# Optimization experiments

Measured on AMD Instinct MI355X. Metric: run time of the kernel, lower is better.

Reference implementation:

```python
import jax, jax.numpy as jnp
import numpy as np

N = 50000      # nodes
E = 800000     # edges (before self-loops)
IN = 256       # in_channels
OUT = 64       # out_channels per head
H = 4          # heads (layer 0)
LEAKY = 0.2    # PyG GATConv negative_slope default


def setup_inputs() -> dict:
    key = jax.random.key(0)
    ks = jax.random.split(key, 16)
    g = 0.1
    inp = {
        "x": jax.random.normal(ks[0], (N, IN), jnp.float32),
        "edge_index": jax.random.randint(ks[1], (2, E), 0, N, dtype=jnp.int32),
        # layer 0: in -> H*OUT, concat=True
        "W0": jax.random.normal(ks[2], (IN, H * OUT), jnp.float32) * g,
        "a_src0": jax.random.normal(ks[3], (H, OUT), jnp.float32) * g,
        "a_dst0": jax.random.normal(ks[4], (H, OUT), jnp.float32) * g,
        "b0": jnp.zeros((H * OUT,), jnp.float32),
        # layer 1: H*OUT -> OUT, heads=1, concat=False
        "W1": jax.random.normal(ks[5], (H * OUT, OUT), jnp.float32) * g,
        "a_src1": jax.random.normal(ks[6], (1, OUT), jnp.float32) * g,
        "a_dst1": jax.random.normal(ks[7], (1, OUT), jnp.float32) * g,
        "b1": jnp.zeros((OUT,), jnp.float32),
        # layer 2: H*OUT -> OUT (input is OUT from layer 1? no: layer1 outputs OUT)
        "W2": jax.random.normal(ks[8], (OUT, OUT), jnp.float32) * g,
        "a_src2": jax.random.normal(ks[9], (1, OUT), jnp.float32) * g,
        "a_dst2": jax.random.normal(ks[10], (1, OUT), jnp.float32) * g,
        "b2": jnp.zeros((OUT,), jnp.float32),
    }
    return inp


def _gat_layer(x, src, dst, W, a_s, a_d, b, heads, concat):
    """PyG GATConv: per-head linear, edge attention logits, segment softmax
    over incoming edges of each destination node, scatter-sum aggregate."""
    n = x.shape[0]
    h = (x @ W).reshape(n, heads, -1)                      # [N, H, C]
    al_s = (h * a_s).sum(-1)                               # [N, H]
    al_d = (h * a_d).sum(-1)                               # [N, H]
    e = jax.nn.leaky_relu(al_s[src] + al_d[dst], LEAKY)    # [E', H]
    m = jax.ops.segment_max(e, dst, num_segments=n)        # [N, H]
    ex = jnp.exp(e - m[dst])
    den = jax.ops.segment_sum(ex, dst, num_segments=n)     # [N, H]
    alpha = ex / (den[dst] + 1e-16)                        # [E', H]
    out = jax.ops.segment_sum(alpha[:, :, None] * h[src], dst, num_segments=n)  # [N,H,C]
    out = out.reshape(n, -1) if concat else out.mean(axis=1)
    return out + b


def reference(x, edge_index, W0, a_src0, a_dst0, b0, W1, a_src1, a_dst1, b1,
              W2, a_src2, a_dst2, b2):
    n = x.shape[0]
    loop = jnp.arange(n, dtype=edge_index.dtype)
    src = jnp.concatenate([edge_index[0], loop])   # PyG add_self_loops=True
    dst = jnp.concatenate([edge_index[1], loop])
    h = _gat_layer(x, src, dst, W0, a_src0, a_dst0, b0, H, True)
    h = jax.nn.elu(h)
    h = _gat_layer(h, src, dst, W1, a_src1, a_dst1, b1, 1, False)
    h = jax.nn.elu(h)
    h = _gat_layer(h, src, dst, W2, a_src2, a_dst2, b2, 1, False)
    h = jax.nn.elu(h)
    return h
```

## Files before the change

### kernel.cpp

```cpp
#include <hip/hip_runtime.h>
#include <hip/hip_bf16.h>


typedef unsigned short ushort_t;
typedef __attribute__((ext_vector_type(8))) short short8;
typedef __attribute__((ext_vector_type(4))) float f32x4;

__device__ __forceinline__ float elu_f(float x){ return x > 0.f ? x : expm1f(x); }
__device__ __forceinline__ float lrelu_f(float x){ return x > 0.f ? x : 0.2f * x; }
__device__ __forceinline__ ushort_t f2b(float f){
  union { float f; unsigned u; } v; v.f = f;
  unsigned r = v.u + 0x7fff + ((v.u >> 16) & 1);
  return (ushort_t)(r >> 16);
}
__device__ __forceinline__ float b2f_lo(unsigned v){
  union { unsigned u; float f; } c; c.u = v << 16; return c.f;
}
__device__ __forceinline__ float b2f_hi(unsigned v){
  union { unsigned u; float f; } c; c.u = v & 0xffff0000u; return c.f;
}

__global__ __launch_bounds__(256) void prep_kernel(const int* __restrict__ ei,
                                                   int* __restrict__ cnt,
                                                   const float4* __restrict__ x4,
                                                   ushort4* __restrict__ xb4, int n4,
                                                   const float* __restrict__ W0,
                                                   ushort_t* __restrict__ W0p,
                                                   const float* __restrict__ W1,
                                                   ushort_t* __restrict__ W1p,
                                                   const float* __restrict__ W2,
                                                   ushort_t* __restrict__ W2p,
                                                   int E, int Etot, int eb, int fb){
  int bid = blockIdx.x; int t = threadIdx.x;
  if(bid < eb){
    int e = bid * 256 + t;
    if(e < Etot){
      int d = (e < E) ? ei[E + e] : (e - E);
      atomicAdd(&cnt[d], 1);
    }
  } else if(bid < eb + fb){
    int i = (bid - eb) * 256 + t;
    if(i < n4){
      float4 v = x4[i];
      ushort4 o;
      o.x = f2b(v.x); o.y = f2b(v.y); o.z = f2b(v.z); o.w = f2b(v.w);
      xb4[i] = o;
    }
  } else {
    int r = bid - eb - fb;
    if(r < 256){
      int i = r * 256 + t; int k = i >> 8, n = i & 255;
      W0p[(size_t)n * 256 + k] = f2b(W0[i]);
    } else if(r < 320){
      int i = (r - 256) * 256 + t; int k = i >> 6, n = i & 63;
      W1p[(size_t)n * 256 + k] = f2b(W1[i]);
    } else {
      int i = (r - 320) * 256 + t; int k = i >> 6, n = i & 63;
      W2p[(size_t)n * 64 + k] = f2b(W2[i]);
    }
  }
}

#define SKP 264
__global__ __launch_bounds__(256) void gemm0_kernel(const ushort_t* __restrict__ A,
                                                    const ushort_t* __restrict__ Bp,
                                                    ushort_t* __restrict__ h0b,
                                                    const float* __restrict__ asrc,
                                                    const float* __restrict__ adst,
                                                    float* __restrict__ als,
                                                    float* __restrict__ ald, int M){
  __shared__ ushort_t As[32 * SKP];
  int t = threadIdx.x;
  int row0 = blockIdx.x * 32;
  {
    int c = t;
    #pragma unroll
    for(int it = 0; it < 4; it++, c += 256){
      int r = c >> 5;
      int kc = (c & 31) << 3;
      int gr = row0 + r;
      short8 v = {};
      if(gr < M) v = *(const short8*)(A + (size_t)gr * 256 + kc);
      *(short8*)(As + r * SKP + kc) = v;
    }
  }
  __syncthreads();
  int wave = t >> 6, lane = t & 63;
  int m = lane & 15, q = lane >> 4;
  int colb = wave;
  const ushort_t* Bq = Bp + (size_t)(colb * 64 + m) * 256 + q * 8;
  const ushort_t* A0 = As + m * SKP + q * 8;
  const ushort_t* A1 = As + (16 + m) * SKP + q * 8;
  f32x4 acc[2][4] = {};
  for(int k0 = 0; k0 < 256; k0 += 32){
    short8 bv[4];
    #pragma unroll
    for(int j = 0; j < 4; j++) bv[j] = *(const short8*)(Bq + (size_t)j * 16 * 256 + k0);
    short8 a0 = *(const short8*)(A0 + k0);
    short8 a1 = *(const short8*)(A1 + k0);
    #pragma unroll
    for(int j = 0; j < 4; j++){
      acc[0][j] = __builtin_amdgcn_mfma_f32_16x16x32_bf16(a0, bv[j], acc[0][j], 0, 0, 0);
      acc[1][j] = __builtin_amdgcn_mfma_f32_16x16x32_bf16(a1, bv[j], acc[1][j], 0, 0, 0);
    }
  }
  #pragma unroll
  for(int rt = 0; rt < 2; rt++){
    #pragma unroll
    for(int j = 0; j < 4; j++){
      int col = colb * 64 + j * 16 + m;
      #pragma unroll
      for(int i = 0; i < 4; i++){
        int gr = row0 + rt * 16 + q * 4 + i;
        if(gr < M) h0b[(size_t)gr * 256 + col] = f2b(acc[rt][j][i]);
      }
    }
    float vs[4] = {0,0,0,0}, vd[4] = {0,0,0,0};
    #pragma unroll
    for(int j = 0; j < 4; j++){
      int col = colb * 64 + j * 16 + m;
      float a_s = asrc[col], a_d = adst[col];
      #pragma unroll
      for(int i = 0; i < 4; i++){
        vs[i] = fmaf(acc[rt][j][i], a_s, vs[i]);
        vd[i] = fmaf(acc[rt][j][i], a_d, vd[i]);
      }
    }
    #pragma unroll
    for(int off = 8; off > 0; off >>= 1){
      #pragma unroll
      for(int i = 0; i < 4; i++){
        vs[i] += __shfl_down(vs[i], off, 16);
        vd[i] += __shfl_down(vd[i], off, 16);
      }
    }
    if(m == 0){
      #pragma unroll
      for(int i = 0; i < 4; i++){
        int gr = row0 + rt * 16 + q * 4 + i;
        if(gr < M){
          als[(size_t)gr * 4 + colb] = vs[i];
          ald[(size_t)gr * 4 + colb] = vd[i];
        }
      }
    }
  }
}

__global__ __launch_bounds__(256) void blocksum_kernel(const int* __restrict__ cnt,
                                                       int* __restrict__ bsum, int N){
  __shared__ int sm[256];
  int t = threadIdx.x;
  int i = blockIdx.x * 256 + t;
  sm[t] = (i < N) ? cnt[i] : 0;
  __syncthreads();
  for(int off = 128; off > 0; off >>= 1){
    if(t < off) sm[t] += sm[t + off];
    __syncthreads();
  }
  if(t == 0) bsum[blockIdx.x] = sm[0];
}

__global__ __launch_bounds__(256) void scanb_kernel(int* __restrict__ bsum, int nb){
  __shared__ int sm[256];
  int t = threadIdx.x;
  int v = (t < nb) ? bsum[t] : 0;
  sm[t] = v;
  __syncthreads();
  for(int off = 1; off < 256; off <<= 1){
    int x = 0;
    if(t >= off) x = sm[t - off];
    __syncthreads();
    sm[t] += x;
    __syncthreads();
  }
  if(t < nb) bsum[t] = sm[t] - v;
}

__global__ __launch_bounds__(256) void scan2_kernel(const int* __restrict__ cnt,
                                                    const int* __restrict__ bsum,
                                                    int* __restrict__ rowptr,
                                                    int* __restrict__ cursor,
                                                    int N, int Etot){
  __shared__ int sm[256];
  int t = threadIdx.x;
  int i = blockIdx.x * 256 + t;
  int v = (i < N) ? cnt[i] : 0;
  sm[t] = v;
  __syncthreads();
  for(int off = 1; off < 256; off <<= 1){
    int x = 0;
    if(t >= off) x = sm[t - off];
    __syncthreads();
    sm[t] += x;
    __syncthreads();
  }
  if(i < N){
    int ex = sm[t] - v + bsum[blockIdx.x];
    rowptr[i] = ex;
    cursor[i] = ex;
    if(i == N - 1) rowptr[N] = Etot;
  }
}

__global__ __launch_bounds__(256) void scatter_kernel(const int* __restrict__ ei,
                                                      int* __restrict__ cursor,
                                                      int* __restrict__ esrc,
                                                      int E, int Etot){
  int e = blockIdx.x * 256 + threadIdx.x;
  if(e >= Etot) return;
  int s, d;
  if(e < E){ s = ei[e]; d = ei[E + e]; } else { s = e - E; d = s; }
  int pos = atomicAdd(&cursor[d], 1);
  esrc[pos] = s;
}

#define H1S 264
__global__ __launch_bounds__(256) void agg0g1_kernel(const int* __restrict__ rowptr,
                                                     const int* __restrict__ esrc,
                                                     const uint2* __restrict__ h0b2,
                                                     const float* __restrict__ als,
                                                     const float* __restrict__ ald,
                                                     const float* __restrict__ b0,
                                                     const ushort_t* __restrict__ W1p,
                                                     const float* __restrict__ as1,
                                                     const float* __restrict__ ad1,
                                                     ushort_t* __restrict__ g1b,
                                                     float* __restrict__ als1,
                                                     float* __restrict__ ald1, int N){
  __shared__ ushort_t Hs[16 * H1S];
  __shared__ float aps[4][16], apd[4][16];
  int t = threadIdx.x;
  int wave = t >> 6, lane = t & 63;
  int nbase = blockIdx.x * 16;
  int h = lane >> 4;
  int mm16 = lane & 15;
  for(int j = 0; j < 4; j++){
    int n = nbase + wave * 4 + j;
    int nl = wave * 4 + j;
    if(n < N){
      int beg = rowptr[n], end = rowptr[n + 1];
      float adh = ald[(size_t)n * 4 + h];
      float4 acc = make_float4(0.f, 0.f, 0.f, 0.f);
      float den = 0.f;
      for(int c0 = beg; c0 < end; c0 += 16){
        int e = c0 + mm16;
        int s = n; float w = 0.f;
        if(e < end){
          s = esrc[e];
          w = expf(lrelu_f(als[(size_t)s * 4 + h] + adh));
        }
        #pragma unroll
        for(int i = 0; i < 16; i++){
          int idx = (lane & 48) + i;
          int si = __shfl(s, idx, 64);
          float wi = __shfl(w, idx, 64);
          uint2 v = h0b2[((size_t)si << 6) + lane];
          acc.x = fmaf(wi, b2f_lo(v.x), acc.x);
          acc.y = fmaf(wi, b2f_hi(v.x), acc.y);
          acc.z = fmaf(wi, b2f_lo(v.y), acc.z);
          acc.w = fmaf(wi, b2f_hi(v.y), acc.w);
          den += wi;
        }
      }
      float inv = 1.f / (den + 1e-16f);
      float4 bb = ((const float4*)b0)[lane];
      uint2 o;
      o.x = (unsigned)f2b(elu_f(acc.x * inv + bb.x)) |
            ((unsigned)f2b(elu_f(acc.y * inv + bb.y)) << 16);
      o.y = (unsigned)f2b(elu_f(acc.z * inv + bb.z)) |
            ((unsigned)f2b(elu_f(acc.w * inv + bb.w)) << 16);
      *(uint2*)(Hs + nl * H1S + lane * 4) = o;
    }
  }
  __syncthreads();
  int m = lane & 15, q = lane >> 4;
  const ushort_t* Bw = W1p + (size_t)(wave * 16 + m) * 256 + q * 8;
  const ushort_t* Aw = Hs + m * H1S + q * 8;
  f32x4 acc = {};
  #pragma unroll
  for(int k0 = 0; k0 < 256; k0 += 32){
    short8 av = *(const short8*)(Aw + k0);
    short8 bv = *(const short8*)(Bw + k0);
    acc = __builtin_amdgcn_mfma_f32_16x16x32_bf16(av, bv, acc, 0, 0, 0);
  }
  float a_s = as1[wave * 16 + m], a_d = ad1[wave * 16 + m];
  float vs[4], vd[4];
  #pragma unroll
  for(int i = 0; i < 4; i++){
    int gn = nbase + q * 4 + i;
    if(gn < N) g1b[(size_t)gn * 64 + wave * 16 + m] = f2b(acc[i]);
    vs[i] = acc[i] * a_s;
    vd[i] = acc[i] * a_d;
  }
  #pragma unroll
  for(int off = 8; off > 0; off >>= 1){
    #pragma unroll
    for(int i = 0; i < 4; i++){
      vs[i] += __shfl_down(vs[i], off, 16);
      vd[i] += __shfl_down(vd[i], off, 16);
    }
  }
  if(m == 0){
    #pragma unroll
    for(int i = 0; i < 4; i++){
      aps[wave][q * 4 + i] = vs[i];
      apd[wave][q * 4 + i] = vd[i];
    }
  }
  __syncthreads();
  if(t < 16){
    int gn = nbase + t;
    if(gn < N){
      als1[gn] = aps[0][t] + aps[1][t] + aps[2][t] + aps[3][t];
      ald1[gn] = apd[0][t] + apd[1][t] + apd[2][t] + apd[3][t];
    }
  }
}

#define H2S 72
__global__ __launch_bounds__(256) void agg1g2_kernel(const int* __restrict__ rowptr,
                                                     const int* __restrict__ esrc,
                                                     const unsigned* __restrict__ g1b,
                                                     const float* __restrict__ als1,
                                                     const float* __restrict__ ald1,
                                                     const float* __restrict__ b1,
                                                     const ushort_t* __restrict__ W2p,
                                                     const float* __restrict__ as2,
                                                     const float* __restrict__ ad2,
                                                     ushort_t* __restrict__ g2b,
                                                     float* __restrict__ als2,
                                                     float* __restrict__ ald2, int N){
  __shared__ ushort_t Hs[16 * H2S];
  __shared__ float aps[4][16], apd[4][16];
  int t = threadIdx.x;
  int wave = t >> 6, lane = t & 63;
  int nbase = blockIdx.x * 16;
  int half = lane >> 5;
  int p = lane & 31;
  for(int j = 0; j < 4; j++){
    int n = nbase + wave * 4 + j;
    int nl = wave * 4 + j;
    if(n < N){
      int beg = rowptr[n], end = rowptr[n + 1];
      float ad = ald1[n];
      float a0 = 0.f, a1 = 0.f, den = 0.f;
      for(int c0 = beg; c0 < end; c0 += 32){
        int e = c0 + p;
        int s = n; float w = 0.f;
        if(e < end){
          s = esrc[e];
          w = expf(lrelu_f(als1[s] + ad));
        }
        #pragma unroll
        for(int i = 0; i < 16; i++){
          int idx = 2 * i + half;
          int si = __shfl(s, idx, 64);
          float wi = __shfl(w, idx, 64);
          unsigned v = g1b[((size_t)si << 5) + p];
          a0 = fmaf(wi, b2f_lo(v), a0);
          a1 = fmaf(wi, b2f_hi(v), a1);
          den += wi;
        }
      }
      a0 += __shfl_xor(a0, 32, 64);
      a1 += __shfl_xor(a1, 32, 64);
      den += __shfl_xor(den, 32, 64);
      float inv = 1.f / (den + 1e-16f);
      float2 bb = ((const float2*)b1)[p];
      if(half == 0){
        unsigned o = (unsigned)f2b(elu_f(a0 * inv + bb.x)) |
                     ((unsigned)f2b(elu_f(a1 * inv + bb.y)) << 16);
        *(unsigned*)(Hs + nl * H2S + p * 2) = o;
      }
    }
  }
  __syncthreads();
  int m = lane & 15, q = lane >> 4;
  const ushort_t* Bw = W2p + (size_t)(wave * 16 + m) * 64 + q * 8;
  const ushort_t* Aw = Hs + m * H2S + q * 8;
  f32x4 acc = {};
  #pragma unroll
  for(int k0 = 0; k0 < 64; k0 += 32){
    short8 av = *(const short8*)(Aw + k0);
    short8 bv = *(const short8*)(Bw + k0);
    acc = __builtin_amdgcn_mfma_f32_16x16x32_bf16(av, bv, acc, 0, 0, 0);
  }
  float a_s = as2[wave * 16 + m], a_d = ad2[wave * 16 + m];
  float vs[4], vd[4];
  #pragma unroll
  for(int i = 0; i < 4; i++){
    int gn = nbase + q * 4 + i;
    if(gn < N) g2b[(size_t)gn * 64 + wave * 16 + m] = f2b(acc[i]);
    vs[i] = acc[i] * a_s;
    vd[i] = acc[i] * a_d;
  }
  #pragma unroll
  for(int off = 8; off > 0; off >>= 1){
    #pragma unroll
    for(int i = 0; i < 4; i++){
      vs[i] += __shfl_down(vs[i], off, 16);
      vd[i] += __shfl_down(vd[i], off, 16);
    }
  }
  if(m == 0){
    #pragma unroll
    for(int i = 0; i < 4; i++){
      aps[wave][q * 4 + i] = vs[i];
      apd[wave][q * 4 + i] = vd[i];
    }
  }
  __syncthreads();
  if(t < 16){
    int gn = nbase + t;
    if(gn < N){
      als2[gn] = aps[0][t] + aps[1][t] + aps[2][t] + aps[3][t];
      ald2[gn] = apd[0][t] + apd[1][t] + apd[2][t] + apd[3][t];
    }
  }
}

__global__ __launch_bounds__(256) void aggF_kernel(const int* __restrict__ rowptr,
                                                   const int* __restrict__ esrc,
                                                   const unsigned* __restrict__ gb,
                                                   const float* __restrict__ als,
                                                   const float* __restrict__ ald,
                                                   const float* __restrict__ b,
                                                   float2* __restrict__ outp, int N){
  int t = threadIdx.x;
  int lane = t & 63;
  int n = blockIdx.x * 4 + (t >> 6);
  if(n >= N) return;
  int half = lane >> 5;
  int p = lane & 31;
  int beg = rowptr[n], end = rowptr[n + 1];
  float ad = ald[n];
  float a0 = 0.f, a1 = 0.f, den = 0.f;
  for(int c0 = beg; c0 < end; c0 += 32){
    int e = c0 + p;
    int s = n; float w = 0.f;
    if(e < end){
      s = esrc[e];
      w = expf(lrelu_f(als[s] + ad));
    }
    #pragma unroll
    for(int i = 0; i < 16; i++){
      int idx = 2 * i + half;
      int si = __shfl(s, idx, 64);
      float wi = __shfl(w, idx, 64);
      unsigned v = gb[((size_t)si << 5) + p];
      a0 = fmaf(wi, b2f_lo(v), a0);
      a1 = fmaf(wi, b2f_hi(v), a1);
      den += wi;
    }
  }
  a0 += __shfl_xor(a0, 32, 64);
  a1 += __shfl_xor(a1, 32, 64);
  den += __shfl_xor(den, 32, 64);
  float inv = 1.f / (den + 1e-16f);
  float2 bb = ((const float2*)b)[p];
  if(half == 0){
    float2 o;
    o.x = elu_f(a0 * inv + bb.x);
    o.y = elu_f(a1 * inv + bb.y);
    outp[((size_t)n << 5) + p] = o;
  }
}

extern "C" void kernel_launch(void* const* d_in, const int* in_sizes, int n_in,
                              void* d_out, int out_size, void* d_ws, size_t ws_size,
                              hipStream_t stream){
  const float* x   = (const float*)d_in[0];
  const int*   ei  = (const int*)d_in[1];
  const float* W0  = (const float*)d_in[2];
  const float* as0 = (const float*)d_in[3];
  const float* ad0 = (const float*)d_in[4];
  const float* b0  = (const float*)d_in[5];
  const float* W1  = (const float*)d_in[6];
  const float* as1 = (const float*)d_in[7];
  const float* ad1 = (const float*)d_in[8];
  const float* b1  = (const float*)d_in[9];
  const float* W2  = (const float*)d_in[10];
  const float* as2 = (const float*)d_in[11];
  const float* ad2 = (const float*)d_in[12];
  const float* b2  = (const float*)d_in[13];
  int N = in_sizes[0] / 256;
  int E = in_sizes[1] / 2;
  int Etot = E + N;

  size_t off = 0;
  auto alc = [&](size_t bytes) -> char* {
    char* p = (char*)d_ws + off;
    off += (bytes + 255) & ~(size_t)255;
    return p;
  };
  ushort_t* xb    = (ushort_t*)alc((size_t)N * 256 * 2);
  ushort_t* h0b   = (ushort_t*)alc((size_t)N * 256 * 2);
  float*    als   = (float*)alc((size_t)N * 4 * 4);
  float*    ald   = (float*)alc((size_t)N * 4 * 4);
  float*    als1  = (float*)alc((size_t)N * 4);
  float*    ald1  = (float*)alc((size_t)N * 4);
  float*    als2  = (float*)alc((size_t)N * 4);
  float*    ald2  = (float*)alc((size_t)N * 4);
  int*      esrc  = (int*)alc((size_t)Etot * 4);
  int*      rowptr= (int*)alc((size_t)(N + 1) * 4);
  int*      cnt   = (int*)alc((size_t)N * 4);
  int*      cursor= (int*)alc((size_t)N * 4);
  int*      bsum  = (int*)alc(256 * 4);
  ushort_t* W0p   = (ushort_t*)alc(256 * 256 * 2);
  ushort_t* W1p   = (ushort_t*)alc(256 * 64 * 2);
  ushort_t* W2p   = (ushort_t*)alc(64 * 64 * 2);

  ushort_t* g1b = xb;
  ushort_t* g2b = h0b;

  int nb = (N + 255) / 256;
  int eb = (Etot + 255) / 256;
  int fb = (N * 64 + 255) / 256;
  int g0b = (N + 31) / 32;
  int tb = (N + 15) / 16;
  int ab = (N + 3) / 4;

  hipMemsetAsync(cnt, 0, (size_t)N * 4, stream);
  prep_kernel<<<eb + fb + 336, 256, 0, stream>>>(ei, cnt, (const float4*)x,
                                                 (ushort4*)xb, N * 64,
                                                 W0, W0p, W1, W1p, W2, W2p,
                                                 E, Etot, eb, fb);
  blocksum_kernel<<<nb, 256, 0, stream>>>(cnt, bsum, N);
  scanb_kernel<<<1, 256, 0, stream>>>(bsum, nb);
  scan2_kernel<<<nb, 256, 0, stream>>>(cnt, bsum, rowptr, cursor, N, Etot);
  scatter_kernel<<<eb, 256, 0, stream>>>(ei, cursor, esrc, E, Etot);

  gemm0_kernel<<<g0b, 256, 0, stream>>>(xb, W0p, h0b, as0, ad0, als, ald, N);

  agg0g1_kernel<<<tb, 256, 0, stream>>>(rowptr, esrc, (const uint2*)h0b,
                                        als, ald, b0, W1p, as1, ad1,
                                        g1b, als1, ald1, N);

  agg1g2_kernel<<<tb, 256, 0, stream>>>(rowptr, esrc, (const unsigned*)g1b,
                                        als1, ald1, b1, W2p, as2, ad2,
                                        g2b, als2, ald2, N);

  aggF_kernel<<<ab, 256, 0, stream>>>(rowptr, esrc, (const unsigned*)g2b,
                                      als2, ald2, b2, (float2*)d_out, N);
}
```

Baseline: 379.2 us.

## Merge graph-build stages into cooperative kernel and split layer-1 aggregation from GEMM

Replaces the memset, prep, blocksum, scan and scatter launches with a single cooperative kernel that uses grid-wide syncs between phases. It also splits the fused layer-0 aggregation plus layer-1 GEMM into two kernels: a one-node-per-wave aggregation that writes bf16 activations to global memory, and a standalone MFMA GEMM that computes the layer-1 attention logits. The aim is to cut launch overhead and give the aggregation better occupancy, without the shared-memory staging and block barriers. In exchange it adds a global round trip for the intermediate activations, plus grid-sync costs in a fixed 512-block grid.

```diff
diff --git a/kernel.cpp b/kernel.cpp
--- a/kernel.cpp
+++ b/kernel.cpp
@@ -1,5 +1,8 @@
 #include <hip/hip_runtime.h>
 #include <hip/hip_bf16.h>
+#include <hip/hip_cooperative_groups.h>
+
+namespace cg = cooperative_groups;
 
 
 typedef unsigned short ushort_t;
@@ -20,44 +23,99 @@
   union { unsigned u; float f; } c; c.u = v & 0xffff0000u; return c.f;
 }
 
-__global__ __launch_bounds__(256) void prep_kernel(const int* __restrict__ ei,
-                                                   int* __restrict__ cnt,
-                                                   const float4* __restrict__ x4,
-                                                   ushort4* __restrict__ xb4, int n4,
-                                                   const float* __restrict__ W0,
-                                                   ushort_t* __restrict__ W0p,
-                                                   const float* __restrict__ W1,
-                                                   ushort_t* __restrict__ W1p,
-                                                   const float* __restrict__ W2,
-                                                   ushort_t* __restrict__ W2p,
-                                                   int E, int Etot, int eb, int fb){
-  int bid = blockIdx.x; int t = threadIdx.x;
-  if(bid < eb){
-    int e = bid * 256 + t;
-    if(e < Etot){
-      int d = (e < E) ? ei[E + e] : (e - E);
-      atomicAdd(&cnt[d], 1);
-    }
-  } else if(bid < eb + fb){
-    int i = (bid - eb) * 256 + t;
-    if(i < n4){
-      float4 v = x4[i];
-      ushort4 o;
-      o.x = f2b(v.x); o.y = f2b(v.y); o.z = f2b(v.z); o.w = f2b(v.w);
-      xb4[i] = o;
-    }
-  } else {
-    int r = bid - eb - fb;
-    if(r < 256){
-      int i = r * 256 + t; int k = i >> 8, n = i & 255;
-      W0p[(size_t)n * 256 + k] = f2b(W0[i]);
-    } else if(r < 320){
-      int i = (r - 256) * 256 + t; int k = i >> 6, n = i & 63;
-      W1p[(size_t)n * 256 + k] = f2b(W1[i]);
-    } else {
-      int i = (r - 320) * 256 + t; int k = i >> 6, n = i & 63;
-      W2p[(size_t)n * 64 + k] = f2b(W2[i]);
-    }
+struct BuildArgs {
+  const int* ei; int* cnt;
+  const float4* x4; ushort4* xb4; int n4;
+  const float* W0; ushort_t* W0p;
+  const float* W1; ushort_t* W1p;
+  const float* W2; ushort_t* W2p;
+  int* bsum; int* rowptr; int* cursor; int* esrc;
+  int N, E, Etot, nb;
+};
+
+__global__ __launch_bounds__(256, 4) void build_kernel(BuildArgs p){
+  cg::grid_group grid = cg::this_grid();
+  __shared__ int sm[256];
+  int t = threadIdx.x;
+  int gid = blockIdx.x * 256 + t;
+  int gsz = gridDim.x * 256;
+  for(int i = gid; i < p.N; i += gsz) p.cnt[i] = 0;
+  for(int i = gid; i < p.n4; i += gsz){
+    float4 v = p.x4[i];
+    ushort4 o;
+    o.x = f2b(v.x); o.y = f2b(v.y); o.z = f2b(v.z); o.w = f2b(v.w);
+    p.xb4[i] = o;
+  }
+  for(int i = gid; i < 256 * 256; i += gsz){
+    int k = i >> 8, n = i & 255;
+    p.W0p[(size_t)n * 256 + k] = f2b(p.W0[i]);
+  }
+  for(int i = gid; i < 256 * 64; i += gsz){
+    int k = i >> 6, n = i & 63;
+    p.W1p[(size_t)n * 256 + k] = f2b(p.W1[i]);
+  }
+  for(int i = gid; i < 64 * 64; i += gsz){
+    int k = i >> 6, n = i & 63;
+    p.W2p[(size_t)n * 64 + k] = f2b(p.W2[i]);
+  }
+  grid.sync();
+  for(int e = gid; e < p.Etot; e += gsz){
+    int d = (e < p.E) ? p.ei[p.E + e] : (e - p.E);
+    atomicAdd(&p.cnt[d], 1);
+  }
+  grid.sync();
+  for(int c = blockIdx.x; c < p.nb; c += gridDim.x){
+    int i = c * 256 + t;
+    sm[t] = (i < p.N) ? p.cnt[i] : 0;
+    __syncthreads();
+    for(int off = 128; off > 0; off >>= 1){
+      if(t < off) sm[t] += sm[t + off];
+      __syncthreads();
+    }
+    if(t == 0) p.bsum[c] = sm[0];
+    __syncthreads();
+  }
+  grid.sync();
+  if(blockIdx.x == 0){
+    int v = (t < p.nb) ? p.bsum[t] : 0;
+    sm[t] = v;
+    __syncthreads();
+    for(int off = 1; off < 256; off <<= 1){
+      int x = 0;
+      if(t >= off) x = sm[t - off];
+      __syncthreads();
+      sm[t] += x;
+      __syncthreads();
+    }
+    if(t < p.nb) p.bsum[t] = sm[t] - v;
+  }
+  grid.sync();
+  for(int c = blockIdx.x; c < p.nb; c += gridDim.x){
+    int i = c * 256 + t;
+    int v = (i < p.N) ? p.cnt[i] : 0;
+    sm[t] = v;
+    __syncthreads();
+    for(int off = 1; off < 256; off <<= 1){
+      int x = 0;
+      if(t >= off) x = sm[t - off];
+      __syncthreads();
+      sm[t] += x;
+      __syncthreads();
+    }
+    if(i < p.N){
+      int ex = sm[t] - v + p.bsum[c];
+      p.rowptr[i] = ex;
+      p.cursor[i] = ex;
+    }
+    __syncthreads();
+  }
+  if(gid == 0) p.rowptr[p.N] = p.Etot;
+  grid.sync();
+  for(int e = gid; e < p.Etot; e += gsz){
+    int s, d;
+    if(e < p.E){ s = p.ei[e]; d = p.ei[p.E + e]; } else { s = e - p.E; d = s; }
+    int pos = atomicAdd(&p.cursor[d], 1);
+    p.esrc[pos] = s;
   }
 }
 
@@ -147,173 +205,125 @@
   }
 }
 
-__global__ __launch_bounds__(256) void blocksum_kernel(const int* __restrict__ cnt,
-                                                       int* __restrict__ bsum, int N){
-  __shared__ int sm[256];
+__global__ __launch_bounds__(256) void agg0_kernel(const int* __restrict__ rowptr,
+                                                   const int* __restrict__ esrc,
+                                                   const uint2* __restrict__ h0b2,
+                                                   const float4* __restrict__ als4,
+                                                   const float4* __restrict__ ald4,
+                                                   const float4* __restrict__ b4,
+                                                   uint2* __restrict__ out2, int N){
   int t = threadIdx.x;
-  int i = blockIdx.x * 256 + t;
-  sm[t] = (i < N) ? cnt[i] : 0;
-  __syncthreads();
-  for(int off = 128; off > 0; off >>= 1){
-    if(t < off) sm[t] += sm[t + off];
-    __syncthreads();
-  }
-  if(t == 0) bsum[blockIdx.x] = sm[0];
-}
-
-__global__ __launch_bounds__(256) void scanb_kernel(int* __restrict__ bsum, int nb){
-  __shared__ int sm[256];
-  int t = threadIdx.x;
-  int v = (t < nb) ? bsum[t] : 0;
-  sm[t] = v;
-  __syncthreads();
-  for(int off = 1; off < 256; off <<= 1){
-    int x = 0;
-    if(t >= off) x = sm[t - off];
-    __syncthreads();
-    sm[t] += x;
-    __syncthreads();
-  }
-  if(t < nb) bsum[t] = sm[t] - v;
-}
-
-__global__ __launch_bounds__(256) void scan2_kernel(const int* __restrict__ cnt,
-                                                    const int* __restrict__ bsum,
-                                                    int* __restrict__ rowptr,
-                                                    int* __restrict__ cursor,
-                                                    int N, int Etot){
-  __shared__ int sm[256];
-  int t = threadIdx.x;
-  int i = blockIdx.x * 256 + t;
-  int v = (i < N) ? cnt[i] : 0;
-  sm[t] = v;
-  __syncthreads();
-  for(int off = 1; off < 256; off <<= 1){
-    int x = 0;
-    if(t >= off) x = sm[t - off];
-    __syncthreads();
-    sm[t] += x;
-    __syncthreads();
-  }
-  if(i < N){
-    int ex = sm[t] - v + bsum[blockIdx.x];
-    rowptr[i] = ex;
-    cursor[i] = ex;
-    if(i == N - 1) rowptr[N] = Etot;
-  }
-}
-
-__global__ __launch_bounds__(256) void scatter_kernel(const int* __restrict__ ei,
-                                                      int* __restrict__ cursor,
-                                                      int* __restrict__ esrc,
-                                                      int E, int Etot){
-  int e = blockIdx.x * 256 + threadIdx.x;
-  if(e >= Etot) return;
-  int s, d;
-  if(e < E){ s = ei[e]; d = ei[E + e]; } else { s = e - E; d = s; }
-  int pos = atomicAdd(&cursor[d], 1);
-  esrc[pos] = s;
-}
-
-#define H1S 264
-__global__ __launch_bounds__(256) void agg0g1_kernel(const int* __restrict__ rowptr,
-                                                     const int* __restrict__ esrc,
-                                                     const uint2* __restrict__ h0b2,
-                                                     const float* __restrict__ als,
-                                                     const float* __restrict__ ald,
-                                                     const float* __restrict__ b0,
-                                                     const ushort_t* __restrict__ W1p,
-                                                     const float* __restrict__ as1,
-                                                     const float* __restrict__ ad1,
-                                                     ushort_t* __restrict__ g1b,
-                                                     float* __restrict__ als1,
-                                                     float* __restrict__ ald1, int N){
-  __shared__ ushort_t Hs[16 * H1S];
-  __shared__ float aps[4][16], apd[4][16];
-  int t = threadIdx.x;
-  int wave = t >> 6, lane = t & 63;
-  int nbase = blockIdx.x * 16;
+  int lane = t & 63;
+  int n = blockIdx.x * 4 + (t >> 6);
+  if(n >= N) return;
   int h = lane >> 4;
-  int mm16 = lane & 15;
-  for(int j = 0; j < 4; j++){
-    int n = nbase + wave * 4 + j;
-    int nl = wave * 4 + j;
-    if(n < N){
-      int beg = rowptr[n], end = rowptr[n + 1];
-      float adh = ald[(size_t)n * 4 + h];
-      float4 acc = make_float4(0.f, 0.f, 0.f, 0.f);
-      float den = 0.f;
-      for(int c0 = beg; c0 < end; c0 += 16){
-        int e = c0 + mm16;
-        int s = n; float w = 0.f;
-        if(e < end){
-          s = esrc[e];
-          w = expf(lrelu_f(als[(size_t)s * 4 + h] + adh));
-        }
-        #pragma unroll
-        for(int i = 0; i < 16; i++){
-          int idx = (lane & 48) + i;
-          int si = __shfl(s, idx, 64);
-          float wi = __shfl(w, idx, 64);
-          uint2 v = h0b2[((size_t)si << 6) + lane];
-          acc.x = fmaf(wi, b2f_lo(v.x), acc.x);
-          acc.y = fmaf(wi, b2f_hi(v.x), acc.y);
-          acc.z = fmaf(wi, b2f_lo(v.y), acc.z);
-          acc.w = fmaf(wi, b2f_hi(v.y), acc.w);
-          den += wi;
-        }
-      }
-      float inv = 1.f / (den + 1e-16f);
-      float4 bb = ((const float4*)b0)[lane];
-      uint2 o;
-      o.x = (unsigned)f2b(elu_f(acc.x * inv + bb.x)) |
-            ((unsigned)f2b(elu_f(acc.y * inv + bb.y)) << 16);
-      o.y = (unsigned)f2b(elu_f(acc.z * inv + bb.z)) |
-            ((unsigned)f2b(elu_f(acc.w * inv + bb.w)) << 16);
-      *(uint2*)(Hs + nl * H1S + lane * 4) = o;
-    }
-  }
-  __syncthreads();
+  int beg = rowptr[n], end = rowptr[n + 1];
+  float adh = ((const float*)(ald4 + n))[h];
+  float4 acc = make_float4(0.f, 0.f, 0.f, 0.f);
+  float den = 0.f;
+  for(int c0 = beg; c0 < end; c0 += 16){
+    int e = c0 + (lane & 15);
+    int s = n; float w = 0.f;
+    if(e < end){
+      s = esrc[e];
+      w = expf(lrelu_f(((const float*)(als4 + s))[h] + adh));
+    }
+    #pragma unroll
+    for(int i = 0; i < 16; i++){
+      int idx = (lane & 48) + i;
+      int si = __shfl(s, idx, 64);
+      float wi = __shfl(w, idx, 64);
+      uint2 v = h0b2[((size_t)si << 6) + lane];
+      acc.x = fmaf(wi, b2f_lo(v.x), acc.x);
+      acc.y = fmaf(wi, b2f_hi(v.x), acc.y);
+      acc.z = fmaf(wi, b2f_lo(v.y), acc.z);
+      acc.w = fmaf(wi, b2f_hi(v.y), acc.w);
+      den += wi;
+    }
+  }
+  float inv = 1.f / (den + 1e-16f);
+  float4 bb = b4[lane];
+  float v0 = elu_f(acc.x * inv + bb.x);
+  float v1 = elu_f(acc.y * inv + bb.y);
+  float v2 = elu_f(acc.z * inv + bb.z);
+  float v3 = elu_f(acc.w * inv + bb.w);
+  uint2 o;
+  o.x = (unsigned)f2b(v0) | ((unsigned)f2b(v1) << 16);
+  o.y = (unsigned)f2b(v2) | ((unsigned)f2b(v3) << 16);
+  out2[((size_t)n << 6) + lane] = o;
+}
+
+__global__ __launch_bounds__(256) void mfma_gemm(const ushort_t* __restrict__ A,
+                                                 const ushort_t* __restrict__ Bp,
+                                                 ushort_t* __restrict__ Cp,
+                                                 const float* __restrict__ asrc,
+                                                 const float* __restrict__ adst,
+                                                 float* __restrict__ als,
+                                                 float* __restrict__ ald,
+                                                 int M, int K, int NC){
+  int wave = threadIdx.x >> 6;
+  int lane = threadIdx.x & 63;
+  int tile0 = (blockIdx.x * 4 + wave) * 2;
+  if(tile0 * 16 >= M) return;
+  bool two = (tile0 + 1) * 16 < M;
   int m = lane & 15, q = lane >> 4;
-  const ushort_t* Bw = W1p + (size_t)(wave * 16 + m) * 256 + q * 8;
-  const ushort_t* Aw = Hs + m * H1S + q * 8;
-  f32x4 acc = {};
+  const ushort_t* Ab = A + (size_t)(tile0 * 16 + m) * K + q * 8;
+  const ushort_t* Bq = Bp + (size_t)m * K + q * 8;
+  f32x4 acc[2][4] = {};
+  for(int k0 = 0; k0 < K; k0 += 32){
+    short8 bv[4];
+    #pragma unroll
+    for(int j = 0; j < 4; j++) bv[j] = *(const short8*)(Bq + (size_t)j * 16 * K + k0);
+    short8 a0 = *(const short8*)(Ab + k0);
+    #pragma unroll
+    for(int j = 0; j < 4; j++)
+      acc[0][j] = __builtin_amdgcn_mfma_f32_16x16x32_bf16(a0, bv[j], acc[0][j], 0, 0, 0);
+    if(two){
+      short8 a1 = *(const short8*)(Ab + (size_t)16 * K + k0);
+      #pragma unroll
+      for(int j = 0; j < 4; j++)
+        acc[1][j] = __builtin_amdgcn_mfma_f32_16x16x32_bf16(a1, bv[j], acc[1][j], 0, 0, 0);
+    }
+  }
   #pragma unroll
-  for(int k0 = 0; k0 < 256; k0 += 32){
-    short8 av = *(const short8*)(Aw + k0);
-    short8 bv = *(const short8*)(Bw + k0);
-    acc = __builtin_amdgcn_mfma_f32_16x16x32_bf16(av, bv, acc, 0, 0, 0);
-  }
-  float a_s = as1[wave * 16 + m], a_d = ad1[wave * 16 + m];
-  float vs[4], vd[4];
-  #pragma unroll
-  for(int i = 0; i < 4; i++){
-    int gn = nbase + q * 4 + i;
-    if(gn < N) g1b[(size_t)gn * 64 + wave * 16 + m] = f2b(acc[i]);
-    vs[i] = acc[i] * a_s;
-    vd[i] = acc[i] * a_d;
-  }
-  #pragma unroll
-  for(int off = 8; off > 0; off >>= 1){
-    #pragma unroll
-    for(int i = 0; i < 4; i++){
-      vs[i] += __shfl_down(vs[i], off, 16);
-      vd[i] += __shfl_down(vd[i], off, 16);
-    }
-  }
-  if(m == 0){
-    #pragma unroll
-    for(int i = 0; i < 4; i++){
-      aps[wave][q * 4 + i] = vs[i];
-      apd[wave][q * 4 + i] = vd[i];
-    }
-  }
-  __syncthreads();
-  if(t < 16){
-    int gn = nbase + t;
-    if(gn < N){
-      als1[gn] = aps[0][t] + aps[1][t] + aps[2][t] + aps[3][t];
-      ald1[gn] = apd[0][t] + apd[1][t] + apd[2][t] + apd[3][t];
+  for(int r = 0; r < 2; r++){
+    if(r == 1 && !two) break;
+    int rowt = tile0 + r;
+    #pragma unroll
+    for(int j = 0; j < 4; j++){
+      int col = j * 16 + m;
+      #pragma unroll
+      for(int i = 0; i < 4; i++){
+        int rr = rowt * 16 + q * 4 + i;
+        Cp[(size_t)rr * NC + col] = f2b(acc[r][j][i]);
+      }
+    }
+    float vs[4] = {0,0,0,0}, vd[4] = {0,0,0,0};
+    #pragma unroll
+    for(int j = 0; j < 4; j++){
+      int col = j * 16 + m;
+      float a_s = asrc[col], a_d = adst[col];
+      #pragma unroll
+      for(int i = 0; i < 4; i++){
+        vs[i] = fmaf(acc[r][j][i], a_s, vs[i]);
+        vd[i] = fmaf(acc[r][j][i], a_d, vd[i]);
+      }
+    }
+    #pragma unroll
+    for(int off = 8; off > 0; off >>= 1){
+      #pragma unroll
+      for(int i = 0; i < 4; i++){
+        vs[i] += __shfl_down(vs[i], off, 16);
+        vd[i] += __shfl_down(vd[i], off, 16);
+      }
+    }
+    if(m == 0){
+      #pragma unroll
+      for(int i = 0; i < 4; i++){
+        int rr = rowt * 16 + q * 4 + i;
+        als[rr] = vs[i];
+        ald[rr] = vd[i];
+      }
     }
   }
 }
@@ -511,31 +521,33 @@
   ushort_t* W1p   = (ushort_t*)alc(256 * 64 * 2);
   ushort_t* W2p   = (ushort_t*)alc(64 * 64 * 2);
 
-  ushort_t* g1b = xb;
-  ushort_t* g2b = h0b;
+  ushort_t* h1b = xb;
+  ushort_t* g1b = h0b;
+  ushort_t* g2b = xb;
 
   int nb = (N + 255) / 256;
-  int eb = (Etot + 255) / 256;
-  int fb = (N * 64 + 255) / 256;
   int g0b = (N + 31) / 32;
+  int rb = ((N / 16) + 7) / 8;
   int tb = (N + 15) / 16;
   int ab = (N + 3) / 4;
 
-  hipMemsetAsync(cnt, 0, (size_t)N * 4, stream);
-  prep_kernel<<<eb + fb + 336, 256, 0, stream>>>(ei, cnt, (const float4*)x,
-                                                 (ushort4*)xb, N * 64,
-                                                 W0, W0p, W1, W1p, W2, W2p,
-                                                 E, Etot, eb, fb);
-  blocksum_kernel<<<nb, 256, 0, stream>>>(cnt, bsum, N);
-  scanb_kernel<<<1, 256, 0, stream>>>(bsum, nb);
-  scan2_kernel<<<nb, 256, 0, stream>>>(cnt, bsum, rowptr, cursor, N, Etot);
-  scatter_kernel<<<eb, 256, 0, stream>>>(ei, cursor, esrc, E, Etot);
+  BuildArgs pa;
+  pa.ei = ei; pa.cnt = cnt;
+  pa.x4 = (const float4*)x; pa.xb4 = (ushort4*)xb; pa.n4 = N * 64;
+  pa.W0 = W0; pa.W0p = W0p; pa.W1 = W1; pa.W1p = W1p; pa.W2 = W2; pa.W2p = W2p;
+  pa.bsum = bsum; pa.rowptr = rowptr; pa.cursor = cursor; pa.esrc = esrc;
+  pa.N = N; pa.E = E; pa.Etot = Etot; pa.nb = nb;
+  void* args[] = { &pa };
+  hipLaunchCooperativeKernel((const void*)build_kernel, dim3(512), dim3(256),
+                             args, 0, stream);
 
   gemm0_kernel<<<g0b, 256, 0, stream>>>(xb, W0p, h0b, as0, ad0, als, ald, N);
-
-  agg0g1_kernel<<<tb, 256, 0, stream>>>(rowptr, esrc, (const uint2*)h0b,
-                                        als, ald, b0, W1p, as1, ad1,
-                                        g1b, als1, ald1, N);
+  agg0_kernel<<<ab, 256, 0, stream>>>(rowptr, esrc, (const uint2*)h0b,
+                                      (const float4*)als, (const float4*)ald,
+                                      (const float4*)b0, (uint2*)h1b, N);
+
+  mfma_gemm<<<rb, 256, 0, stream>>>(h1b, W1p, g1b, as1, ad1, als1, ald1,
+                                    N, 256, 64);
 
   agg1g2_kernel<<<tb, 256, 0, stream>>>(rowptr, esrc, (const unsigned*)g1b,
                                         als1, ald1, b1, W2p, as2, ad2,
```

New measurement: 697.1 us. +83.8%, slower.
